# Kernel optimization log

Hardware: AMD Instinct MI355X
Metric: run time of the kernel (lower is better)

The kernel has to match this reference:

```python
import jax, jax.numpy as jnp
import numpy as np

SIZE, H, W = 2048, 64, 64


def setup_inputs() -> dict:
    key = jax.random.key(0)
    k1, k2 = jax.random.split(key)
    inp = jax.random.uniform(k1, (SIZE, 1, H, W), dtype=jnp.float32)
    # learnable Sobel kernel, initialized as in the module (sobel / 2, tiled per multiplier)
    sobel = jnp.asarray([1.0, 0.0, -1.0, 2.0, 0.0, -2.0, 1.0, 0.0, -1.0], dtype=jnp.float32) / 2.0
    weight = sobel[None, :]                    # (n_mult=1, 9)
    weight_factor = jnp.asarray([2.0], dtype=jnp.float32)
    scale = jnp.ones((1, 1), dtype=jnp.float32)
    return {"input": inp, "weight": weight, "weight_factor": weight_factor, "scale": scale}


def _conv3x3(x, k):
    # x: [B,1,H,W], k: [1,1,3,3], padding 1, stride 1
    return jax.lax.conv_general_dilated(
        x, k, window_strides=(1, 1), padding=[(1, 1), (1, 1)],
        dimension_numbers=("NCHW", "OIHW", "NCHW"))


def reference(input, weight, weight_factor, scale):
    # single multiplier branch (mul_approx_func_arr=[1]); mul_wrapper emulated as exact multiply
    wc = jnp.clip(weight, -1.0, 1.0)[0]                # hardtanh(weight, -1, 1), branch 0 -> (9,)
    wf = jnp.clip(weight_factor, 1.0, 255.0)           # hardtanh(weight_factor, 1, 255) -> (1,)
    wr = (wc * wf).reshape(3, 3)
    k = wr[None, None]                                  # (1,1,3,3)
    kt = wr.T[None, None]
    gx = _conv3x3(input, k)
    gy = _conv3x3(input, kt)
    g = jnp.abs(gx) + jnp.abs(gy)                       # [B,1,H,W]
    b = g.shape[0]
    gflat = g.reshape(b, -1)
    gmin = gflat.min(axis=1).reshape(-1, 1, 1, 1)
    gmax = gflat.max(axis=1).reshape(-1, 1, 1, 1)
    dx = jnp.clip(gmax - gmin, 1.0, None)
    norm = (g - gmin) / dx * 255.0                      # accurate path (grad path)
    val = jnp.floor(norm)                               # approx path value (x.data = x_data)
    x = norm + jax.lax.stop_gradient(val - norm)        # straight-through value swap
    x = x / jax.lax.stop_gradient(scale[0])             # divide by scale[ii].data (detached)
    return x[None]                                      # stack over mult_list (len 1) -> [1,B,1,H,W]
```

## Files before the change

### kernel.cpp

```cpp
#include <hip/hip_runtime.h>

typedef float vf4 __attribute__((ext_vector_type(4)));

__global__ __launch_bounds__(256, 6) void sobel_v5(
    const float* __restrict__ in,
    const float* __restrict__ weight,
    const float* __restrict__ wfac_p,
    const float* __restrict__ scale_p,
    float* __restrict__ out)
{
    __shared__ float smin[4], smax[4];

    const int tid = threadIdx.x;
    const int img = blockIdx.x;
    const float* __restrict__ src = in + (size_t)img * 4096;
    float* __restrict__ dst = out + (size_t)img * 4096;

    const float wf = fminf(fmaxf(wfac_p[0], 1.0f), 255.0f);
    float wr[9];
#pragma unroll
    for (int i = 0; i < 9; ++i)
        wr[i] = fminf(fmaxf(weight[i], -1.0f), 1.0f) * wf;
    const float invscale = 1.0f / scale_p[0];

    const int c = tid & 15;
    const int R = tid >> 4;

    vf4 m[6];
#pragma unroll
    for (int k = 0; k < 6; ++k) {
        const int rr = 4 * R - 1 + k;
        const int rrc = min(max(rr, 0), 63);
        m[k] = *(const vf4*)(src + rrc * 64 + 4 * c);
    }

    float w6[6][6];
#pragma unroll
    for (int k = 0; k < 6; ++k) {
        const int rr = 4 * R - 1 + k;
        const bool rv = (rr >= 0) & (rr < 64);
        float lft = __shfl_up(m[k].w, 1, 16);
        float rgt = __shfl_down(m[k].x, 1, 16);
        lft = (c == 0)  ? 0.0f : lft;
        rgt = (c == 15) ? 0.0f : rgt;
        w6[k][0] = rv ? lft     : 0.0f;
        w6[k][1] = rv ? m[k].x  : 0.0f;
        w6[k][2] = rv ? m[k].y  : 0.0f;
        w6[k][3] = rv ? m[k].z  : 0.0f;
        w6[k][4] = rv ? m[k].w  : 0.0f;
        w6[k][5] = rv ? rgt     : 0.0f;
    }

    float g[4][4];
    float gmn = __builtin_inff(), gmx = -__builtin_inff();
#pragma unroll
    for (int i = 0; i < 4; ++i) {
#pragma unroll
        for (int j = 0; j < 4; ++j) {
            float gx = 0.0f, gy = 0.0f;
#pragma unroll
            for (int dr = 0; dr < 3; ++dr) {
#pragma unroll
                for (int dc = 0; dc < 3; ++dc) {
                    const float a = w6[i + dr][j + dc];
                    gx = fmaf(a, wr[dr * 3 + dc], gx);
                    gy = fmaf(a, wr[dc * 3 + dr], gy);
                }
            }
            const float gv = fabsf(gx) + fabsf(gy);
            g[i][j] = gv;
            gmn = fminf(gmn, gv);
            gmx = fmaxf(gmx, gv);
        }
    }

#pragma unroll
    for (int off = 32; off > 0; off >>= 1) {
        gmn = fminf(gmn, __shfl_xor(gmn, off));
        gmx = fmaxf(gmx, __shfl_xor(gmx, off));
    }
    if ((tid & 63) == 0) { smin[tid >> 6] = gmn; smax[tid >> 6] = gmx; }
    __syncthreads();
    gmn = fminf(fminf(smin[0], smin[1]), fminf(smin[2], smin[3]));
    gmx = fmaxf(fmaxf(smax[0], smax[1]), fmaxf(smax[2], smax[3]));

    const float inv = 255.0f / fmaxf(gmx - gmn, 1.0f);

#pragma unroll
    for (int i = 0; i < 4; ++i) {
        vf4 o;
        o.x = floorf((g[i][0] - gmn) * inv) * invscale;
        o.y = floorf((g[i][1] - gmn) * inv) * invscale;
        o.z = floorf((g[i][2] - gmn) * inv) * invscale;
        o.w = floorf((g[i][3] - gmn) * inv) * invscale;
        __builtin_nontemporal_store(o, (vf4*)&dst[(4 * R + i) * 64 + 4 * c]);
    }
}

extern "C" void kernel_launch(void* const* d_in, const int* in_sizes, int n_in,
                              void* d_out, int out_size, void* d_ws, size_t ws_size,
                              hipStream_t stream) {
    const float* inp   = (const float*)d_in[0];
    const float* wgt   = (const float*)d_in[1];
    const float* wfac  = (const float*)d_in[2];
    const float* scale = (const float*)d_in[3];
    float* out = (float*)d_out;

    sobel_v5<<<2048, 256, 0, stream>>>(inp, wgt, wfac, scale, out);
}
```

Baseline: 14.50 us.

## Process two images per block and prefetch the second during the first

```diff
diff --git a/kernel.cpp b/kernel.cpp
--- a/kernel.cpp
+++ b/kernel.cpp
@@ -2,19 +2,17 @@
 
 typedef float vf4 __attribute__((ext_vector_type(4)));
 
-__global__ __launch_bounds__(256, 6) void sobel_v5(
+__global__ __launch_bounds__(256, 4) void sobel_v6(
     const float* __restrict__ in,
     const float* __restrict__ weight,
     const float* __restrict__ wfac_p,
     const float* __restrict__ scale_p,
     float* __restrict__ out)
 {
-    __shared__ float smin[4], smax[4];
+    __shared__ float smin[2][4], smax[2][4];
 
     const int tid = threadIdx.x;
-    const int img = blockIdx.x;
-    const float* __restrict__ src = in + (size_t)img * 4096;
-    float* __restrict__ dst = out + (size_t)img * 4096;
+    const int img0 = blockIdx.x * 2;
 
     const float wf = fminf(fmaxf(wfac_p[0], 1.0f), 255.0f);
     float wr[9];
@@ -25,13 +23,17 @@
 
     const int c = tid & 15;
     const int R = tid >> 4;
+    const int wv = tid >> 6;
+
+    const float* __restrict__ src0 = in + (size_t)img0 * 4096;
+    const float* __restrict__ src1 = src0 + 4096;
 
     vf4 m[6];
 #pragma unroll
     for (int k = 0; k < 6; ++k) {
         const int rr = 4 * R - 1 + k;
         const int rrc = min(max(rr, 0), 63);
-        m[k] = *(const vf4*)(src + rrc * 64 + 4 * c);
+        m[k] = *(const vf4*)(src0 + rrc * 64 + 4 * c);
     }
 
     float w6[6][6];
@@ -43,12 +45,20 @@
         float rgt = __shfl_down(m[k].x, 1, 16);
         lft = (c == 0)  ? 0.0f : lft;
         rgt = (c == 15) ? 0.0f : rgt;
-        w6[k][0] = rv ? lft     : 0.0f;
-        w6[k][1] = rv ? m[k].x  : 0.0f;
-        w6[k][2] = rv ? m[k].y  : 0.0f;
-        w6[k][3] = rv ? m[k].z  : 0.0f;
-        w6[k][4] = rv ? m[k].w  : 0.0f;
-        w6[k][5] = rv ? rgt     : 0.0f;
+        w6[k][0] = rv ? lft    : 0.0f;
+        w6[k][1] = rv ? m[k].x : 0.0f;
+        w6[k][2] = rv ? m[k].y : 0.0f;
+        w6[k][3] = rv ? m[k].z : 0.0f;
+        w6[k][4] = rv ? m[k].w : 0.0f;
+        w6[k][5] = rv ? rgt    : 0.0f;
+    }
+
+    vf4 m2[6];
+#pragma unroll
+    for (int k = 0; k < 6; ++k) {
+        const int rr = 4 * R - 1 + k;
+        const int rrc = min(max(rr, 0), 63);
+        m2[k] = *(const vf4*)(src1 + rrc * 64 + 4 * c);
     }
 
     float g[4][4];
@@ -79,21 +89,85 @@
         gmn = fminf(gmn, __shfl_xor(gmn, off));
         gmx = fmaxf(gmx, __shfl_xor(gmx, off));
     }
-    if ((tid & 63) == 0) { smin[tid >> 6] = gmn; smax[tid >> 6] = gmx; }
+    if ((tid & 63) == 0) { smin[0][wv] = gmn; smax[0][wv] = gmx; }
     __syncthreads();
-    gmn = fminf(fminf(smin[0], smin[1]), fminf(smin[2], smin[3]));
-    gmx = fmaxf(fmaxf(smax[0], smax[1]), fmaxf(smax[2], smax[3]));
+    gmn = fminf(fminf(smin[0][0], smin[0][1]), fminf(smin[0][2], smin[0][3]));
+    gmx = fmaxf(fmaxf(smax[0][0], smax[0][1]), fmaxf(smax[0][2], smax[0][3]));
 
-    const float inv = 255.0f / fmaxf(gmx - gmn, 1.0f);
+    {
+        const float inv = 255.0f / fmaxf(gmx - gmn, 1.0f);
+        float* __restrict__ dst = out + (size_t)img0 * 4096;
+#pragma unroll
+        for (int i = 0; i < 4; ++i) {
+            vf4 o;
+            o.x = floorf((g[i][0] - gmn) * inv) * invscale;
+            o.y = floorf((g[i][1] - gmn) * inv) * invscale;
+            o.z = floorf((g[i][2] - gmn) * inv) * invscale;
+            o.w = floorf((g[i][3] - gmn) * inv) * invscale;
+            __builtin_nontemporal_store(o, (vf4*)&dst[(4 * R + i) * 64 + 4 * c]);
+        }
+    }
 
 #pragma unroll
+    for (int k = 0; k < 6; ++k) {
+        const int rr = 4 * R - 1 + k;
+        const bool rv = (rr >= 0) & (rr < 64);
+        float lft = __shfl_up(m2[k].w, 1, 16);
+        float rgt = __shfl_down(m2[k].x, 1, 16);
+        lft = (c == 0)  ? 0.0f : lft;
+        rgt = (c == 15) ? 0.0f : rgt;
+        w6[k][0] = rv ? lft     : 0.0f;
+        w6[k][1] = rv ? m2[k].x : 0.0f;
+        w6[k][2] = rv ? m2[k].y : 0.0f;
+        w6[k][3] = rv ? m2[k].z : 0.0f;
+        w6[k][4] = rv ? m2[k].w : 0.0f;
+        w6[k][5] = rv ? rgt     : 0.0f;
+    }
+
+    gmn = __builtin_inff(); gmx = -__builtin_inff();
+#pragma unroll
     for (int i = 0; i < 4; ++i) {
-        vf4 o;
-        o.x = floorf((g[i][0] - gmn) * inv) * invscale;
-        o.y = floorf((g[i][1] - gmn) * inv) * invscale;
-        o.z = floorf((g[i][2] - gmn) * inv) * invscale;
-        o.w = floorf((g[i][3] - gmn) * inv) * invscale;
-        __builtin_nontemporal_store(o, (vf4*)&dst[(4 * R + i) * 64 + 4 * c]);
+#pragma unroll
+        for (int j = 0; j < 4; ++j) {
+            float gx = 0.0f, gy = 0.0f;
+#pragma unroll
+            for (int dr = 0; dr < 3; ++dr) {
+#pragma unroll
+                for (int dc = 0; dc < 3; ++dc) {
+                    const float a = w6[i + dr][j + dc];
+                    gx = fmaf(a, wr[dr * 3 + dc], gx);
+                    gy = fmaf(a, wr[dc * 3 + dr], gy);
+                }
+            }
+            const float gv = fabsf(gx) + fabsf(gy);
+            g[i][j] = gv;
+            gmn = fminf(gmn, gv);
+            gmx = fmaxf(gmx, gv);
+        }
+    }
+
+#pragma unroll
+    for (int off = 32; off > 0; off >>= 1) {
+        gmn = fminf(gmn, __shfl_xor(gmn, off));
+        gmx = fmaxf(gmx, __shfl_xor(gmx, off));
+    }
+    if ((tid & 63) == 0) { smin[1][wv] = gmn; smax[1][wv] = gmx; }
+    __syncthreads();
+    gmn = fminf(fminf(smin[1][0], smin[1][1]), fminf(smin[1][2], smin[1][3]));
+    gmx = fmaxf(fmaxf(smax[1][0], smax[1][1]), fmaxf(smax[1][2], smax[1][3]));
+
+    {
+        const float inv = 255.0f / fmaxf(gmx - gmn, 1.0f);
+        float* __restrict__ dst = out + (size_t)(img0 + 1) * 4096;
+#pragma unroll
+        for (int i = 0; i < 4; ++i) {
+            vf4 o;
+            o.x = floorf((g[i][0] - gmn) * inv) * invscale;
+            o.y = floorf((g[i][1] - gmn) * inv) * invscale;
+            o.z = floorf((g[i][2] - gmn) * inv) * invscale;
+            o.w = floorf((g[i][3] - gmn) * inv) * invscale;
+            __builtin_nontemporal_store(o, (vf4*)&dst[(4 * R + i) * 64 + 4 * c]);
+        }
     }
 }
 
@@ -106,5 +180,5 @@
     const float* scale = (const float*)d_in[3];
     float* out = (float*)d_out;
 
-    sobel_v5<<<2048, 256, 0, stream>>>(inp, wgt, wfac, scale, out);
+    sobel_v6<<<1024, 256, 0, stream>>>(inp, wgt, wfac, scale, out);
 }
```

After: 14.45 us. About the same (-0.3%).
